# Optimization experiments

Measured on AMD Instinct MI355X. Metric: run time of the kernel, lower is better.

The kernel has to match this reference:

```python
import jax, jax.numpy as jnp
import numpy as np

NUM_CLASSES = 40
EOS_COEF = 0.1
IGNORE = 255
W_CLASS, W_MASK, W_DICE = 2.0, 5.0, 5.0
EPS = 1e-8


def setup_inputs() -> dict:
    key = jax.random.key(0)
    k1, k2, k3, k4 = jax.random.split(key, 4)
    B, Q, H, W = 4, 100, 256, 256
    pred_logits = jax.random.normal(k1, (B, Q, NUM_CLASSES + 1), dtype=jnp.float32)
    pred_masks = jax.random.normal(k2, (B, Q, H, W), dtype=jnp.float32)
    targets = jax.random.randint(k3, (B, H, W), 0, NUM_CLASSES)
    ign = jax.random.uniform(k4, (B, H, W)) < 0.05
    targets = jnp.where(ign, IGNORE, targets).astype(jnp.int32)
    return {"pred_logits": pred_logits, "pred_masks": pred_masks, "targets": targets}


def reference(pred_logits, pred_masks, targets):
    B, Q, _ = pred_logits.shape
    C = NUM_CLASSES
    f32 = jnp.float32
    valid = targets != IGNORE                      # [B,H,W]
    tgt_safe = jnp.where(valid, targets, 0)        # in-range for indexing

    # ---- loss_labels: pixel->query assignment, per-query mode label ----
    # sigmoid is monotone, so argmax over queries of raw logits == argmax of sigmoid
    assign = jnp.argmax(pred_masks, axis=1)        # [B,H,W]
    b_idx = jnp.broadcast_to(jnp.arange(B)[:, None, None], targets.shape)
    # counts[b,q,c] = #valid pixels assigned to query q with label c
    counts = jnp.zeros((B, Q, C), f32).at[b_idx, assign, tgt_safe].add(valid.astype(f32))
    has_pix = counts.sum(-1) > 0                   # [B,Q]
    # mode = argmax of counts (ties -> smallest class, matching torch.mode)
    target_classes = jnp.where(has_pix, jnp.argmax(counts, axis=-1), C)  # [B,Q]

    logp = jax.nn.log_softmax(pred_logits, axis=-1)                      # [B,Q,C+1]
    nll = -jnp.take_along_axis(logp, target_classes[..., None], axis=-1)[..., 0]
    empty_weight = jnp.ones(C + 1, f32).at[-1].set(EOS_COEF)
    # ignore_index = num_classes in the CE over classes
    ce = jnp.where(target_classes != C, nll * empty_weight[target_classes], 0.0)
    p = jnp.exp(-ce)
    loss_ce = jnp.mean((1.0 - p) ** 2 * ce)

    # ---- loss_masks: per-pixel CE over queries + per-class dice ----
    logp_pix = jax.nn.log_softmax(pred_masks, axis=1)                    # [B,Q,H,W]
    nll_pix = -jnp.take_along_axis(logp_pix, tgt_safe[:, None], axis=1)[:, 0]  # [B,H,W]
    n_valid = valid.astype(f32).sum()
    ce_mask = jnp.sum(jnp.where(valid, nll_pix, 0.0)) / jnp.maximum(n_valid, 1.0)

    sig = jax.nn.sigmoid(pred_masks)                                     # [B,Q,H,W]
    tmask = (targets[:, None] == jnp.arange(C)[None, :, None, None]).astype(f32)  # [B,C,H,W]
    vm = valid[:, None].astype(f32)                                      # [B,1,H,W]
    inter = jnp.einsum('bqhw,bchw->bqc', sig, tmask * vm)                # numerator uses valid mask
    src_sum = sig.sum(axis=(2, 3))                                       # [B,Q]
    tsum = tmask.sum(axis=(2, 3))                                        # [B,C]
    dice = 2.0 * inter / (src_sum[:, :, None] + tsum[:, None, :] + EPS)  # [B,Q,C]
    present = tsum.sum(axis=0) > 0                                       # [C]
    dice_loss = jnp.sum(jnp.where(present, 1.0 - dice.mean(axis=(0, 1)), 0.0)) / C

    combined = W_MASK * ce_mask + W_DICE * dice_loss
    return W_CLASS * loss_ce + combined
```

## Files before the change

kernel.cpp:

```cpp
#include <hip/hip_runtime.h>

constexpr int B = 4, Q = 100, C = 40, Cp1 = 41, HW = 65536;

constexpr int FBLKS = 512;

constexpr int WS_WORDS = 32562;

typedef __attribute__((ext_vector_type(8))) short short8;
typedef __attribute__((ext_vector_type(4))) float f32x4;

__device__ __forceinline__ short f2bf(float f) {
    unsigned u = __float_as_uint(f);
    u += 0x7FFF + ((u >> 16) & 1);
    return (short)(u >> 16);
}

__global__ void kZ(unsigned* __restrict__ ws, int n) {
    int i = blockIdx.x * blockDim.x + threadIdx.x;
    for (; i < n; i += gridDim.x * blockDim.x) ws[i] = 0u;
}

__global__ __launch_bounds__(256) void kF(const float* __restrict__ masks,
                                          const int* __restrict__ targets,
                                          unsigned* __restrict__ counts,
                                          unsigned* __restrict__ tsum,
                                          float* __restrict__ ce_sum,
                                          unsigned* __restrict__ n_valid,
                                          float* __restrict__ inter_ext) {
    __shared__ __align__(16) short tileS[16 * 512];
    __shared__ __align__(8) unsigned char tgt8[512];
    __shared__ float smem[160];

    const int tid = threadIdx.x;
    const int l = tid & 63, w = tid >> 6;
    const int m = l & 15, quad = l >> 4;

    const int blk = blockIdx.x;
    const int b = blk >> 7;
    const int seg = blk & 127;
    const int pxb = w * 128 + 2 * l;
    const int p0 = seg * 512 + pxb;

    const int2 tg = *(const int2*)(targets + (size_t)b * HW + p0);
    *(unsigned short*)&tgt8[pxb] =
        (unsigned short)((tg.x & 255) | ((tg.y & 255) << 8));
    unsigned* ts_local = (unsigned*)&smem[0];
    if (tid < C) ts_local[tid] = 0u;
    __syncthreads();

    const float* mp = masks + (size_t)b * Q * HW + p0;
    const int tg0 = tg.x, tg1 = tg.y;

    float m20 = -INFINITY, m21 = -INFINITY;
    float s0 = 0.f, s1 = 0.f, xt0 = 0.f, xt1 = 0.f;
    int am0 = 0, am1 = 0;

    char* tbytes = (char*)tileS;
    const int wbase = w * 256 + l * 4;

    const int colbase = w * 16;
    const int cv = (w == 2) ? ((m == 8) ? 255 : 32 + m) : (colbase + m);

    for (int qt = 0; qt < 7; ++qt) {
        const int nu = (qt == 6) ? 4 : 16;

        float2 vv[16];
        const float* mq = mp + (size_t)(qt * 16) * HW;
        #pragma unroll
        for (int u = 0; u < 16; ++u)
            if (u < nu) vv[u] = *(const float2*)(mq + (size_t)u * HW);

        #pragma unroll
        for (int u = 0; u < 16; ++u)
            if (u < nu) {
                const int q = qt * 16 + u;
                const float v0 = vv[u].x, v1 = vv[u].y;
                s0 += __expf(v0);
                s1 += __expf(v1);
                am0 = (v0 > m20) ? q : am0;  m20 = fmaxf(m20, v0);
                am1 = (v1 > m21) ? q : am1;  m21 = fmaxf(m21, v1);
                xt0 = (q == tg0) ? v0 : xt0;
                xt1 = (q == tg1) ? v1 : xt1;
                const float g0 = __builtin_amdgcn_rcpf(1.f + __expf(-v0));
                const float g1 = __builtin_amdgcn_rcpf(1.f + __expf(-v1));
                const unsigned pk = (unsigned)(unsigned short)f2bf(g0) |
                                    ((unsigned)(unsigned short)f2bf(g1) << 16);
                *(unsigned*)(tbytes + ((u * 1024 + wbase) ^ ((u & 7) << 4))) = pk;
            }

        asm volatile("s_waitcnt lgkmcnt(0)" ::: "memory");
        __builtin_amdgcn_s_barrier();
        asm volatile("" ::: "memory");

        f32x4 acc = {0.f, 0.f, 0.f, 0.f};
        if (w < 3) {
            #pragma unroll
            for (int kc = 0; kc < 16; ++kc) {
                const short8 av = *(const short8*)(tbytes +
                    ((m * 1024 + kc * 64 + quad * 16) ^ ((m & 7) << 4)));
                const unsigned long long tw =
                    *(const unsigned long long*)&tgt8[kc * 32 + quad * 8];
                short8 bv;
                #pragma unroll
                for (int j = 0; j < 8; ++j) {
                    const int tb = (int)((tw >> (8 * j)) & 255);
                    bv[j] = (tb == cv) ? (short)0x3F80 : (short)0;
                }
                acc = __builtin_amdgcn_mfma_f32_16x16x32_bf16(av, bv, acc, 0, 0, 0);
            }
        }
        asm volatile("" ::: "memory");
        __builtin_amdgcn_s_barrier();
        asm volatile("" ::: "memory");

        if (w < 3 && !(w == 2 && m > 8)) {
            #pragma unroll
            for (int reg = 0; reg < 4; ++reg) {
                const int q = qt * 16 + quad * 4 + reg;
                if (q < 100)
                    atomicAdd(&inter_ext[(size_t)(b * Q + q) * Cp1 + colbase + m],
                              acc[reg]);
            }
        }
    }

    float ce = 0.f;
    unsigned nv = 0u;
    if (tg0 != 255) {
        ce += __logf(s0) - xt0; nv++;
        atomicAdd(&counts[((size_t)b * Q + am0) * C + tg0], 1u);
        atomicAdd(&ts_local[tg0], 1u);
    }
    if (tg1 != 255) {
        ce += __logf(s1) - xt1; nv++;
        atomicAdd(&counts[((size_t)b * Q + am1) * C + tg1], 1u);
        atomicAdd(&ts_local[tg1], 1u);
    }
    for (int off = 32; off; off >>= 1) {
        ce += __shfl_xor(ce, off);
        nv += __shfl_xor(nv, off);
    }
    float* cred = &smem[64];
    unsigned* vred = (unsigned*)&smem[72];
    if (l == 0) { cred[w] = ce; vred[w] = nv; }
    __syncthreads();
    if (tid == 0) {
        atomicAdd(ce_sum, cred[0] + cred[1] + cred[2] + cred[3]);
        atomicAdd(n_valid, vred[0] + vred[1] + vred[2] + vred[3]);
    }
    if (tid < C) {
        unsigned t = ts_local[tid];
        if (t) atomicAdd(&tsum[b * C + tid], t);
    }
}

__global__ __launch_bounds__(512) void kC(const float* __restrict__ logits,
                                          const unsigned* __restrict__ counts,
                                          const unsigned* __restrict__ tsum,
                                          const float* __restrict__ inter_ext,
                                          const float* __restrict__ ce_sum,
                                          const unsigned* __restrict__ n_valid,
                                          float* __restrict__ out) {
    int tid = threadIdx.x;
    __shared__ float dice_sum[C];
    __shared__ float ssum[B * Q];
    __shared__ float wred[8];
    __shared__ float s_lce;
    if (tid < C) dice_sum[tid] = 0.f;
    if (tid < B * Q) {
        const float* r = inter_ext + (size_t)tid * Cp1;
        float t = 0.f;
        #pragma unroll
        for (int c = 0; c < Cp1; ++c) t += r[c];
        ssum[tid] = t;
    }

    float ce_acc = 0.f;
    for (int i = tid; i < B * Q; i += 512) {
        const unsigned* cnt = counts + (size_t)i * C;
        unsigned best = 0;
        int tc = C;
        #pragma unroll
        for (int c = 0; c < C; ++c) {
            unsigned v = cnt[c];
            if (v > best) { best = v; tc = c; }
        }
        if (tc != C) {
            const float* lg = logits + (size_t)i * Cp1;
            float mm = -INFINITY, xt = 0.f;
            #pragma unroll
            for (int c = 0; c < Cp1; ++c) {
                float v = lg[c];
                mm = fmaxf(mm, v);
                if (c == tc) xt = v;
            }
            float ss = 0.f;
            #pragma unroll
            for (int c = 0; c < Cp1; ++c) ss += __expf(lg[c] - mm);
            float nll = mm + __logf(ss) - xt;
            float p = __expf(-nll);
            float om = 1.f - p;
            ce_acc += om * om * nll;
        }
    }
    for (int off = 32; off; off >>= 1) ce_acc += __shfl_xor(ce_acc, off);
    if ((tid & 63) == 0) wred[tid >> 6] = ce_acc;
    __syncthreads();
    if (tid == 0) {
        float t = 0.f;
        for (int w = 0; w < 8; ++w) t += wred[w];
        s_lce = t;
    }

    for (int i = tid; i < B * Q * C; i += 512) {
        int bq = i / C, c = i - bq * C;
        float denom = ssum[bq] + (float)tsum[(bq / Q) * C + c] + 1e-8f;
        atomicAdd(&dice_sum[c], 2.f * inter_ext[(size_t)bq * Cp1 + c] / denom);
    }
    __syncthreads();

    if (tid == 0) {
        float dl = 0.f;
        for (int c = 0; c < C; ++c) {
            unsigned ts = tsum[c] + tsum[C + c] + tsum[2 * C + c] + tsum[3 * C + c];
            if (ts > 0) dl += 1.f - dice_sum[c] * (1.f / (B * Q));
        }
        dl *= (1.f / C);
        float ce_mask = ce_sum[0] / fmaxf((float)n_valid[0], 1.f);
        float lce = s_lce * (1.f / (B * Q));
        out[0] = 2.f * lce + 5.f * ce_mask + 5.f * dl;
    }
}

extern "C" void kernel_launch(void* const* d_in, const int* in_sizes, int n_in,
                              void* d_out, int out_size, void* d_ws, size_t ws_size,
                              hipStream_t stream) {
    const float* logits  = (const float*)d_in[0];
    const float* masks   = (const float*)d_in[1];
    const int*   targets = (const int*)d_in[2];
    float* out = (float*)d_out;

    unsigned* ws        = (unsigned*)d_ws;
    unsigned* counts    = ws;
    unsigned* tsum      = ws + 16000;
    float*    ce_sum    = (float*)(ws + 16160);
    unsigned* n_valid   = ws + 16161;
    float*    inter_ext = (float*)(ws + 16162);

    kZ<<<64, 256, 0, stream>>>(ws, WS_WORDS);
    kF<<<FBLKS, 256, 0, stream>>>(masks, targets, counts, tsum, ce_sum, n_valid,
                                  inter_ext);
    kC<<<1, 512, 0, stream>>>(logits, counts, tsum, inter_ext, ce_sum, n_valid, out);
}
```

Before: 220.7 us.

## Precompute one-hot target tile in LDS and double-buffer mask loads

Replaces the per-iteration one-hot B-operand construction from packed target bytes with a one-hot bf16 matrix built once in shared memory (48 rows by 512 pixels, swizzled), so the MFMA loop reads B directly from LDS. It also prefetches the next 16 queries' mask values into a second register buffer while the current chunk is processed, and adds a launch-bounds occupancy hint of 2. The cost is about 48KB of extra LDS per block and doubled register usage for the prefetch buffers, which may limit occupancy or cause spills.

Result: slower. 233.2 us (+5.7%).

```diff
diff --git a/kernel.cpp b/kernel.cpp
--- a/kernel.cpp
+++ b/kernel.cpp
@@ -20,15 +20,15 @@
     for (; i < n; i += gridDim.x * blockDim.x) ws[i] = 0u;
 }
 
-__global__ __launch_bounds__(256) void kF(const float* __restrict__ masks,
-                                          const int* __restrict__ targets,
-                                          unsigned* __restrict__ counts,
-                                          unsigned* __restrict__ tsum,
-                                          float* __restrict__ ce_sum,
-                                          unsigned* __restrict__ n_valid,
-                                          float* __restrict__ inter_ext) {
+__global__ __launch_bounds__(256, 2) void kF(const float* __restrict__ masks,
+                                             const int* __restrict__ targets,
+                                             unsigned* __restrict__ counts,
+                                             unsigned* __restrict__ tsum,
+                                             float* __restrict__ ce_sum,
+                                             unsigned* __restrict__ n_valid,
+                                             float* __restrict__ inter_ext) {
     __shared__ __align__(16) short tileS[16 * 512];
-    __shared__ __align__(8) unsigned char tgt8[512];
+    __shared__ __align__(16) short oneh[48 * 512];
     __shared__ float smem[160];
 
     const int tid = threadIdx.x;
@@ -42,39 +42,65 @@
     const int p0 = seg * 512 + pxb;
 
     const int2 tg = *(const int2*)(targets + (size_t)b * HW + p0);
-    *(unsigned short*)&tgt8[pxb] =
-        (unsigned short)((tg.x & 255) | ((tg.y & 255) << 8));
+    const int tg0 = tg.x, tg1 = tg.y;
+
+    const float* mp = masks + (size_t)b * Q * HW + p0;
+
+    float2 vv0[16], vv1[16];
+    #pragma unroll
+    for (int u = 0; u < 16; ++u)
+        vv0[u] = *(const float2*)(mp + (size_t)u * HW);
+
     unsigned* ts_local = (unsigned*)&smem[0];
+    {
+        int4 z = {0, 0, 0, 0};
+        int4* o4 = (int4*)oneh;
+        #pragma unroll
+        for (int i = 0; i < 12; ++i) o4[tid + i * 256] = z;
+    }
     if (tid < C) ts_local[tid] = 0u;
-    __syncthreads();
-
-    const float* mp = masks + (size_t)b * Q * HW + p0;
-    const int tg0 = tg.x, tg1 = tg.y;
+    asm volatile("s_waitcnt lgkmcnt(0)" ::: "memory");
+    __builtin_amdgcn_s_barrier();
+    asm volatile("" ::: "memory");
+    {
+        const int r0 = (tg0 == 255) ? 40 : tg0;
+        const int r1 = (tg1 == 255) ? 40 : tg1;
+        *(short*)((char*)oneh + r0 * 1024 + ((2 * pxb) ^ ((r0 & 7) << 4))) =
+            (short)0x3F80;
+        *(short*)((char*)oneh + r1 * 1024 + ((2 * pxb + 2) ^ ((r1 & 7) << 4))) =
+            (short)0x3F80;
+    }
+    asm volatile("s_waitcnt lgkmcnt(0)" ::: "memory");
+    __builtin_amdgcn_s_barrier();
+    asm volatile("" ::: "memory");
 
     float m20 = -INFINITY, m21 = -INFINITY;
     float s0 = 0.f, s1 = 0.f, xt0 = 0.f, xt1 = 0.f;
     int am0 = 0, am1 = 0;
 
-    char* tbytes = (char*)tileS;
+    char* tb = (char*)tileS;
+    char* ob = (char*)oneh;
     const int wbase = w * 256 + l * 4;
-
     const int colbase = w * 16;
-    const int cv = (w == 2) ? ((m == 8) ? 255 : 32 + m) : (colbase + m);
-
+    const int brow = colbase + m;
+
+    #pragma unroll
     for (int qt = 0; qt < 7; ++qt) {
         const int nu = (qt == 6) ? 4 : 16;
 
-        float2 vv[16];
-        const float* mq = mp + (size_t)(qt * 16) * HW;
-        #pragma unroll
-        for (int u = 0; u < 16; ++u)
-            if (u < nu) vv[u] = *(const float2*)(mq + (size_t)u * HW);
+        if (qt < 6) {
+            const int nn = (qt == 5) ? 4 : 16;
+            const float* mq = mp + (size_t)((qt + 1) * 16) * HW;
+            #pragma unroll
+            for (int u = 0; u < 16; ++u)
+                if (u < nn) vv1[u] = *(const float2*)(mq + (size_t)u * HW);
+        }
 
         #pragma unroll
         for (int u = 0; u < 16; ++u)
             if (u < nu) {
                 const int q = qt * 16 + u;
-                const float v0 = vv[u].x, v1 = vv[u].y;
+                const float v0 = vv0[u].x, v1 = vv0[u].y;
                 s0 += __expf(v0);
                 s1 += __expf(v1);
                 am0 = (v0 > m20) ? q : am0;  m20 = fmaxf(m20, v0);
@@ -85,7 +111,7 @@
                 const float g1 = __builtin_amdgcn_rcpf(1.f + __expf(-v1));
                 const unsigned pk = (unsigned)(unsigned short)f2bf(g0) |
                                     ((unsigned)(unsigned short)f2bf(g1) << 16);
-                *(unsigned*)(tbytes + ((u * 1024 + wbase) ^ ((u & 7) << 4))) = pk;
+                *(unsigned*)(tb + ((u * 1024 + wbase) ^ ((u & 7) << 4))) = pk;
             }
 
         asm volatile("s_waitcnt lgkmcnt(0)" ::: "memory");
@@ -96,20 +122,14 @@
         if (w < 3) {
             #pragma unroll
             for (int kc = 0; kc < 16; ++kc) {
-                const short8 av = *(const short8*)(tbytes +
+                const short8 av = *(const short8*)(tb +
                     ((m * 1024 + kc * 64 + quad * 16) ^ ((m & 7) << 4)));
-                const unsigned long long tw =
-                    *(const unsigned long long*)&tgt8[kc * 32 + quad * 8];
-                short8 bv;
-                #pragma unroll
-                for (int j = 0; j < 8; ++j) {
-                    const int tb = (int)((tw >> (8 * j)) & 255);
-                    bv[j] = (tb == cv) ? (short)0x3F80 : (short)0;
-                }
+                const short8 bv = *(const short8*)(ob +
+                    ((brow * 1024 + kc * 64 + quad * 16) ^ ((brow & 7) << 4)));
                 acc = __builtin_amdgcn_mfma_f32_16x16x32_bf16(av, bv, acc, 0, 0, 0);
             }
         }
-        asm volatile("" ::: "memory");
+        asm volatile("s_waitcnt lgkmcnt(0)" ::: "memory");
         __builtin_amdgcn_s_barrier();
         asm volatile("" ::: "memory");
 
@@ -122,6 +142,9 @@
                               acc[reg]);
             }
         }
+
+        #pragma unroll
+        for (int u = 0; u < 16; ++u) vv0[u] = vv1[u];
     }
 
     float ce = 0.f;
```

## Restructure mask kernel to single-wave blocks with register double-buffered loads

Applied to the files above, without the earlier changes.

Each block becomes a single 64-thread wave handling 128 pixels. That wave computes all three class tiles with MFMA itself, so the per-tile block barriers go away. The next 16 query rows are prefetched into registers while the current tile is processed, and the one-hot target operands are precomputed once. The cost is four times as many blocks, which quadruples the global float atomics into the intersection buffer and raises register pressure.

After: 359.4 us. 1.63x slower.

```diff
diff --git a/kernel.cpp b/kernel.cpp
--- a/kernel.cpp
+++ b/kernel.cpp
@@ -2,7 +2,7 @@
 
 constexpr int B = 4, Q = 100, C = 40, Cp1 = 41, HW = 65536;
 
-constexpr int FBLKS = 512;
+constexpr int FBLKS = 2048;
 
 constexpr int WS_WORDS = 32562;
 
@@ -20,61 +20,81 @@
     for (; i < n; i += gridDim.x * blockDim.x) ws[i] = 0u;
 }
 
-__global__ __launch_bounds__(256) void kF(const float* __restrict__ masks,
-                                          const int* __restrict__ targets,
-                                          unsigned* __restrict__ counts,
-                                          unsigned* __restrict__ tsum,
-                                          float* __restrict__ ce_sum,
-                                          unsigned* __restrict__ n_valid,
-                                          float* __restrict__ inter_ext) {
-    __shared__ __align__(16) short tileS[16 * 512];
-    __shared__ __align__(8) unsigned char tgt8[512];
-    __shared__ float smem[160];
-
-    const int tid = threadIdx.x;
-    const int l = tid & 63, w = tid >> 6;
+__global__ __launch_bounds__(64, 2) void kF(const float* __restrict__ masks,
+                                            const int* __restrict__ targets,
+                                            unsigned* __restrict__ counts,
+                                            unsigned* __restrict__ tsum,
+                                            float* __restrict__ ce_sum,
+                                            unsigned* __restrict__ n_valid,
+                                            float* __restrict__ inter_ext) {
+    __shared__ __align__(16) short tileS[16 * 128];
+    __shared__ __align__(8) unsigned char tgt8[128];
+    __shared__ unsigned ts_local[C];
+
+    const int l = threadIdx.x;
     const int m = l & 15, quad = l >> 4;
 
     const int blk = blockIdx.x;
-    const int b = blk >> 7;
-    const int seg = blk & 127;
-    const int pxb = w * 128 + 2 * l;
-    const int p0 = seg * 512 + pxb;
+    const int b = blk >> 9;
+    const int seg = blk & 511;
+    const int pxb = 2 * l;
+    const int p0 = seg * 128 + pxb;
 
     const int2 tg = *(const int2*)(targets + (size_t)b * HW + p0);
+    const int tg0 = tg.x, tg1 = tg.y;
     *(unsigned short*)&tgt8[pxb] =
-        (unsigned short)((tg.x & 255) | ((tg.y & 255) << 8));
-    unsigned* ts_local = (unsigned*)&smem[0];
-    if (tid < C) ts_local[tid] = 0u;
+        (unsigned short)((tg0 & 255) | ((tg1 & 255) << 8));
+    if (l < C) ts_local[l] = 0u;
     __syncthreads();
 
     const float* mp = masks + (size_t)b * Q * HW + p0;
-    const int tg0 = tg.x, tg1 = tg.y;
+
+    float2 vvA[16], vvB[16];
+    #pragma unroll
+    for (int u = 0; u < 16; ++u)
+        vvA[u] = *(const float2*)(mp + (size_t)u * HW);
+
+    short8 bv[3][4];
+    #pragma unroll
+    for (int ct = 0; ct < 3; ++ct) {
+        const int cv = (ct == 2 && m == 8) ? 255 : (ct * 16 + m);
+        #pragma unroll
+        for (int kc = 0; kc < 4; ++kc) {
+            const unsigned long long tw =
+                *(const unsigned long long*)&tgt8[kc * 32 + quad * 8];
+            short8 v;
+            #pragma unroll
+            for (int j = 0; j < 8; ++j)
+                v[j] = ((int)((tw >> (8 * j)) & 255) == cv) ? (short)0x3F80
+                                                            : (short)0;
+            bv[ct][kc] = v;
+        }
+    }
 
     float m20 = -INFINITY, m21 = -INFINITY;
     float s0 = 0.f, s1 = 0.f, xt0 = 0.f, xt1 = 0.f;
     int am0 = 0, am1 = 0;
 
-    char* tbytes = (char*)tileS;
-    const int wbase = w * 256 + l * 4;
-
-    const int colbase = w * 16;
-    const int cv = (w == 2) ? ((m == 8) ? 255 : 32 + m) : (colbase + m);
-
+    char* tb = (char*)tileS;
+    const int wrbase = 4 * l;
+
+    #pragma unroll
     for (int qt = 0; qt < 7; ++qt) {
         const int nu = (qt == 6) ? 4 : 16;
 
-        float2 vv[16];
-        const float* mq = mp + (size_t)(qt * 16) * HW;
-        #pragma unroll
-        for (int u = 0; u < 16; ++u)
-            if (u < nu) vv[u] = *(const float2*)(mq + (size_t)u * HW);
+        if (qt < 6) {
+            const int nn = (qt == 5) ? 4 : 16;
+            const float* mq = mp + (size_t)((qt + 1) * 16) * HW;
+            #pragma unroll
+            for (int u = 0; u < 16; ++u)
+                if (u < nn) vvB[u] = *(const float2*)(mq + (size_t)u * HW);
+        }
 
         #pragma unroll
         for (int u = 0; u < 16; ++u)
             if (u < nu) {
                 const int q = qt * 16 + u;
-                const float v0 = vv[u].x, v1 = vv[u].y;
+                const float v0 = vvA[u].x, v1 = vvA[u].y;
                 s0 += __expf(v0);
                 s1 += __expf(v1);
                 am0 = (v0 > m20) ? q : am0;  m20 = fmaxf(m20, v0);
@@ -85,43 +105,32 @@
                 const float g1 = __builtin_amdgcn_rcpf(1.f + __expf(-v1));
                 const unsigned pk = (unsigned)(unsigned short)f2bf(g0) |
                                     ((unsigned)(unsigned short)f2bf(g1) << 16);
-                *(unsigned*)(tbytes + ((u * 1024 + wbase) ^ ((u & 7) << 4))) = pk;
-            }
-
-        asm volatile("s_waitcnt lgkmcnt(0)" ::: "memory");
-        __builtin_amdgcn_s_barrier();
-        asm volatile("" ::: "memory");
-
-        f32x4 acc = {0.f, 0.f, 0.f, 0.f};
-        if (w < 3) {
-            #pragma unroll
-            for (int kc = 0; kc < 16; ++kc) {
-                const short8 av = *(const short8*)(tbytes +
-                    ((m * 1024 + kc * 64 + quad * 16) ^ ((m & 7) << 4)));
-                const unsigned long long tw =
-                    *(const unsigned long long*)&tgt8[kc * 32 + quad * 8];
-                short8 bv;
+                *(unsigned*)(tb + ((u * 256 + wrbase) ^ ((u & 7) << 4))) = pk;
+            }
+
+        #pragma unroll
+        for (int ct = 0; ct < 3; ++ct) {
+            f32x4 acc = {0.f, 0.f, 0.f, 0.f};
+            #pragma unroll
+            for (int kc = 0; kc < 4; ++kc) {
+                const short8 av = *(const short8*)(tb +
+                    ((m * 256 + kc * 64 + quad * 16) ^ ((m & 7) << 4)));
+                acc = __builtin_amdgcn_mfma_f32_16x16x32_bf16(av, bv[ct][kc],
+                                                              acc, 0, 0, 0);
+            }
+            if (!(ct == 2 && m > 8)) {
                 #pragma unroll
-                for (int j = 0; j < 8; ++j) {
-                    const int tb = (int)((tw >> (8 * j)) & 255);
-                    bv[j] = (tb == cv) ? (short)0x3F80 : (short)0;
+                for (int reg = 0; reg < 4; ++reg) {
+                    const int q = qt * 16 + quad * 4 + reg;
+                    if (q < 100)
+                        atomicAdd(&inter_ext[(size_t)(b * Q + q) * Cp1 +
+                                             ct * 16 + m], acc[reg]);
                 }
-                acc = __builtin_amdgcn_mfma_f32_16x16x32_bf16(av, bv, acc, 0, 0, 0);
-            }
-        }
-        asm volatile("" ::: "memory");
-        __builtin_amdgcn_s_barrier();
-        asm volatile("" ::: "memory");
-
-        if (w < 3 && !(w == 2 && m > 8)) {
-            #pragma unroll
-            for (int reg = 0; reg < 4; ++reg) {
-                const int q = qt * 16 + quad * 4 + reg;
-                if (q < 100)
-                    atomicAdd(&inter_ext[(size_t)(b * Q + q) * Cp1 + colbase + m],
-                              acc[reg]);
-            }
-        }
+            }
+        }
+
+        #pragma unroll
+        for (int u = 0; u < 16; ++u) vvA[u] = vvB[u];
     }
 
     float ce = 0.f;
@@ -140,17 +149,14 @@
         ce += __shfl_xor(ce, off);
         nv += __shfl_xor(nv, off);
     }
-    float* cred = &smem[64];
-    unsigned* vred = (unsigned*)&smem[72];
-    if (l == 0) { cred[w] = ce; vred[w] = nv; }
-    __syncthreads();
-    if (tid == 0) {
-        atomicAdd(ce_sum, cred[0] + cred[1] + cred[2] + cred[3]);
-        atomicAdd(n_valid, vred[0] + vred[1] + vred[2] + vred[3]);
-    }
-    if (tid < C) {
-        unsigned t = ts_local[tid];
-        if (t) atomicAdd(&tsum[b * C + tid], t);
+    if (l == 0) {
+        atomicAdd(ce_sum, ce);
+        atomicAdd(n_valid, nv);
+    }
+    __syncthreads();
+    if (l < C) {
+        unsigned t = ts_local[l];
+        if (t) atomicAdd(&tsum[b * C + l], t);
     }
 }
 
@@ -248,7 +254,7 @@
     float*    inter_ext = (float*)(ws + 16162);
 
     kZ<<<64, 256, 0, stream>>>(ws, WS_WORDS);
-    kF<<<FBLKS, 256, 0, stream>>>(masks, targets, counts, tsum, ce_sum, n_valid,
-                                  inter_ext);
+    kF<<<FBLKS, 64, 0, stream>>>(masks, targets, counts, tsum, ce_sum, n_valid,
+                                 inter_ext);
     kC<<<1, 512, 0, stream>>>(logits, counts, tsum, inter_ext, ce_sum, n_valid, out);
 }
```

## Use one pixel per thread with 512-thread blocks and double-buffered tile

Applied to the files above, without the earlier changes.

The fused kernel moves from 256 threads handling two pixels each to 512 threads handling one pixel each. This doubles the warps available to hide memory latency. The shared sigmoid tile is double-buffered across query tiles, so the second barrier per tile is dropped and a single __syncthreads remains. In exchange, global loads shrink from float2 to scalar floats, shared stores become 16-bit, and only 3 of 8 warps run the MFMA stage, leaving more warps idle during it.

After: 212.9 us. 3.6% less time.

```diff
diff --git a/kernel.cpp b/kernel.cpp
--- a/kernel.cpp
+++ b/kernel.cpp
@@ -20,16 +20,18 @@
     for (; i < n; i += gridDim.x * blockDim.x) ws[i] = 0u;
 }
 
-__global__ __launch_bounds__(256) void kF(const float* __restrict__ masks,
+__global__ __launch_bounds__(512) void kF(const float* __restrict__ masks,
                                           const int* __restrict__ targets,
                                           unsigned* __restrict__ counts,
                                           unsigned* __restrict__ tsum,
                                           float* __restrict__ ce_sum,
                                           unsigned* __restrict__ n_valid,
                                           float* __restrict__ inter_ext) {
-    __shared__ __align__(16) short tileS[16 * 512];
+    __shared__ __align__(16) short tileS[2][16 * 512];
     __shared__ __align__(8) unsigned char tgt8[512];
-    __shared__ float smem[160];
+    __shared__ unsigned ts_local[C];
+    __shared__ float cred[8];
+    __shared__ unsigned vred[8];
 
     const int tid = threadIdx.x;
     const int l = tid & 63, w = tid >> 6;
@@ -38,115 +40,93 @@
     const int blk = blockIdx.x;
     const int b = blk >> 7;
     const int seg = blk & 127;
-    const int pxb = w * 128 + 2 * l;
-    const int p0 = seg * 512 + pxb;
-
-    const int2 tg = *(const int2*)(targets + (size_t)b * HW + p0);
-    *(unsigned short*)&tgt8[pxb] =
-        (unsigned short)((tg.x & 255) | ((tg.y & 255) << 8));
-    unsigned* ts_local = (unsigned*)&smem[0];
+    const int p0 = seg * 512 + tid;
+
+    const int tgv = targets[(size_t)b * HW + p0];
+    tgt8[tid] = (unsigned char)(tgv & 255);
     if (tid < C) ts_local[tid] = 0u;
-    __syncthreads();
 
     const float* mp = masks + (size_t)b * Q * HW + p0;
-    const int tg0 = tg.x, tg1 = tg.y;
-
-    float m20 = -INFINITY, m21 = -INFINITY;
-    float s0 = 0.f, s1 = 0.f, xt0 = 0.f, xt1 = 0.f;
-    int am0 = 0, am1 = 0;
-
-    char* tbytes = (char*)tileS;
-    const int wbase = w * 256 + l * 4;
-
-    const int colbase = w * 16;
-    const int cv = (w == 2) ? ((m == 8) ? 255 : 32 + m) : (colbase + m);
+
+    float m2 = -INFINITY, s = 0.f, xt = 0.f;
+    int am = 0;
+
+    const int cv = (w == 2 && m == 8) ? 255 : (w * 16 + m);
 
     for (int qt = 0; qt < 7; ++qt) {
+        char* tbq = (char*)(&tileS[qt & 1][0]);
         const int nu = (qt == 6) ? 4 : 16;
 
-        float2 vv[16];
-        const float* mq = mp + (size_t)(qt * 16) * HW;
+        float vv[16];
         #pragma unroll
         for (int u = 0; u < 16; ++u)
-            if (u < nu) vv[u] = *(const float2*)(mq + (size_t)u * HW);
+            if (u < nu) vv[u] = mp[(size_t)(qt * 16 + u) * HW];
 
         #pragma unroll
         for (int u = 0; u < 16; ++u)
             if (u < nu) {
                 const int q = qt * 16 + u;
-                const float v0 = vv[u].x, v1 = vv[u].y;
-                s0 += __expf(v0);
-                s1 += __expf(v1);
-                am0 = (v0 > m20) ? q : am0;  m20 = fmaxf(m20, v0);
-                am1 = (v1 > m21) ? q : am1;  m21 = fmaxf(m21, v1);
-                xt0 = (q == tg0) ? v0 : xt0;
-                xt1 = (q == tg1) ? v1 : xt1;
-                const float g0 = __builtin_amdgcn_rcpf(1.f + __expf(-v0));
-                const float g1 = __builtin_amdgcn_rcpf(1.f + __expf(-v1));
-                const unsigned pk = (unsigned)(unsigned short)f2bf(g0) |
-                                    ((unsigned)(unsigned short)f2bf(g1) << 16);
-                *(unsigned*)(tbytes + ((u * 1024 + wbase) ^ ((u & 7) << 4))) = pk;
-            }
-
-        asm volatile("s_waitcnt lgkmcnt(0)" ::: "memory");
-        __builtin_amdgcn_s_barrier();
-        asm volatile("" ::: "memory");
-
-        f32x4 acc = {0.f, 0.f, 0.f, 0.f};
+                const float v = vv[u];
+                s += __expf(v);
+                am = (v > m2) ? q : am;
+                m2 = fmaxf(m2, v);
+                xt = (q == tgv) ? v : xt;
+                const float g = __builtin_amdgcn_rcpf(1.f + __expf(-v));
+                *(short*)(tbq + ((u * 1024 + 2 * tid) ^ ((u & 7) << 4))) =
+                    f2bf(g);
+            }
+
+        __syncthreads();
+
         if (w < 3) {
+            f32x4 acc = {0.f, 0.f, 0.f, 0.f};
             #pragma unroll
             for (int kc = 0; kc < 16; ++kc) {
-                const short8 av = *(const short8*)(tbytes +
+                const short8 av = *(const short8*)(tbq +
                     ((m * 1024 + kc * 64 + quad * 16) ^ ((m & 7) << 4)));
                 const unsigned long long tw =
                     *(const unsigned long long*)&tgt8[kc * 32 + quad * 8];
                 short8 bv;
                 #pragma unroll
-                for (int j = 0; j < 8; ++j) {
-                    const int tb = (int)((tw >> (8 * j)) & 255);
-                    bv[j] = (tb == cv) ? (short)0x3F80 : (short)0;
+                for (int j = 0; j < 8; ++j)
+                    bv[j] = ((int)((tw >> (8 * j)) & 255) == cv)
+                                ? (short)0x3F80 : (short)0;
+                acc = __builtin_amdgcn_mfma_f32_16x16x32_bf16(av, bv, acc,
+                                                              0, 0, 0);
+            }
+            if (!(w == 2 && m > 8)) {
+                #pragma unroll
+                for (int reg = 0; reg < 4; ++reg) {
+                    const int q = qt * 16 + quad * 4 + reg;
+                    if (q < 100)
+                        atomicAdd(&inter_ext[(size_t)(b * Q + q) * Cp1 +
+                                             w * 16 + m], acc[reg]);
                 }
-                acc = __builtin_amdgcn_mfma_f32_16x16x32_bf16(av, bv, acc, 0, 0, 0);
-            }
-        }
-        asm volatile("" ::: "memory");
-        __builtin_amdgcn_s_barrier();
-        asm volatile("" ::: "memory");
-
-        if (w < 3 && !(w == 2 && m > 8)) {
-            #pragma unroll
-            for (int reg = 0; reg < 4; ++reg) {
-                const int q = qt * 16 + quad * 4 + reg;
-                if (q < 100)
-                    atomicAdd(&inter_ext[(size_t)(b * Q + q) * Cp1 + colbase + m],
-                              acc[reg]);
             }
         }
     }
 
     float ce = 0.f;
     unsigned nv = 0u;
-    if (tg0 != 255) {
-        ce += __logf(s0) - xt0; nv++;
-        atomicAdd(&counts[((size_t)b * Q + am0) * C + tg0], 1u);
-        atomicAdd(&ts_local[tg0], 1u);
-    }
-    if (tg1 != 255) {
-        ce += __logf(s1) - xt1; nv++;
-        atomicAdd(&counts[((size_t)b * Q + am1) * C + tg1], 1u);
-        atomicAdd(&ts_local[tg1], 1u);
+    if (tgv != 255) {
+        ce = __logf(s) - xt;
+        nv = 1u;
+        atomicAdd(&counts[((size_t)b * Q + am) * C + tgv], 1u);
+        atomicAdd(&ts_local[tgv], 1u);
     }
     for (int off = 32; off; off >>= 1) {
         ce += __shfl_xor(ce, off);
         nv += __shfl_xor(nv, off);
     }
-    float* cred = &smem[64];
-    unsigned* vred = (unsigned*)&smem[72];
     if (l == 0) { cred[w] = ce; vred[w] = nv; }
     __syncthreads();
     if (tid == 0) {
-        atomicAdd(ce_sum, cred[0] + cred[1] + cred[2] + cred[3]);
-        atomicAdd(n_valid, vred[0] + vred[1] + vred[2] + vred[3]);
+        float t = 0.f;
+        unsigned n = 0u;
+        #pragma unroll
+        for (int i = 0; i < 8; ++i) { t += cred[i]; n += vred[i]; }
+        atomicAdd(ce_sum, t);
+        atomicAdd(n_valid, n);
     }
     if (tid < C) {
         unsigned t = ts_local[tid];
@@ -248,7 +228,7 @@
     float*    inter_ext = (float*)(ws + 16162);
 
     kZ<<<64, 256, 0, stream>>>(ws, WS_WORDS);
-    kF<<<FBLKS, 256, 0, stream>>>(masks, targets, counts, tsum, ce_sum, n_valid,
+    kF<<<FBLKS, 512, 0, stream>>>(masks, targets, counts, tsum, ce_sum, n_valid,
                                   inter_ext);
     kC<<<1, 512, 0, stream>>>(logits, counts, tsum, inter_ext, ce_sum, n_valid, out);
 }
```
